# Kernel tuning notes

Hardware: AMD Instinct MI355X
Metric: run time of the kernel (lower is better)

Reference implementation:

```python
import jax, jax.numpy as jnp
import numpy as np

ROUTING_ITERS = 3


def _squash(x):
    # scale = |x|^2 / (1+|x|^2) ; out = scale * x / |x|  (matches torch module exactly)
    squared_norm = jnp.sum(x * x, axis=-1, keepdims=True)
    scale = squared_norm / (1.0 + squared_norm)
    return scale * x / jnp.sqrt(squared_norm)


def setup_inputs() -> dict:
    key = jax.random.key(0)
    k1, k2 = jax.random.split(key)
    B, NODES, CIN = 64, 6272, 8
    CAPS, COUT = 10, 16
    x = jax.random.normal(k1, (B, NODES, CIN), dtype=jnp.float32)
    W = jax.random.normal(k2, (CAPS, NODES, CIN, COUT), dtype=jnp.float32)
    return {"x": x, "W": W}


def reference(x, W):
    # u_hat: [B, caps, nodes, 1, out]  (the torch code's per-node 1x8 @ 8x16 matmul)
    u_hat = jnp.einsum('bni,cnio->bcno', x, W)[:, :, :, None, :]
    b_ij = jnp.zeros_like(u_hat)
    v_j = None
    for it in range(ROUTING_ITERS):
        c_ij = jax.nn.softmax(b_ij, axis=2)  # softmax over nodes dim (dim=2)
        s_j = jnp.sum(c_ij * u_hat, axis=2, keepdims=True)  # [B,caps,1,1,out]
        v_j = _squash(s_j)
        if it < ROUTING_ITERS - 1:
            a_ij = jnp.sum(u_hat * v_j, axis=-1, keepdims=True)  # agreement
            b_ij = b_ij + a_ij  # broadcasts over the out dim, as in torch
    return jnp.squeeze(v_j, axis=3)  # [B, caps, 1, out]
```

## Files before the change

### kernel.cpp

```cpp
#include <hip/hip_runtime.h>
#include <math.h>

#define NODES 6272
#define BATCH 64
#define NCAPS 10
#define CIN   8
#define COUT  16
#define NWB   16
#define NWW   4
#define CHUNKS (NODES / NWB)
#define PART_STRIDE 20

__global__ __launch_bounds__(256) void k_xpose(const float* __restrict__ x,
                                               float* __restrict__ xT) {
    int g = blockIdx.x * 256 + threadIdx.x;
    int b = g & 63;
    int n = g >> 6;
    const float* xp = x + (size_t)b * (NODES * CIN) + (size_t)n * CIN;
    float4 a0 = *reinterpret_cast<const float4*>(xp);
    float4 a1 = *reinterpret_cast<const float4*>(xp + 4);
    float4* op = reinterpret_cast<float4*>(xT + (size_t)g * 8);
    op[0] = a0;
    op[1] = a1;
}

template<int PASS>
__global__ __launch_bounds__(256) void k_pass(const float* __restrict__ xT,
                                              const float* __restrict__ W,
                                              const float* __restrict__ vsum,
                                              float* __restrict__ part) {
    __shared__ float Wl[NWB * 128];
    __shared__ float Rbuf[2][64][PART_STRIDE];

    int bid  = blockIdx.x;
    int wid  = threadIdx.x >> 6;
    int lane = threadIdx.x & 63;
    int c    = bid % NCAPS;
    int ch   = bid / NCAPS;
    int n0   = ch * NWB;

    {
        const float4* src = reinterpret_cast<const float4*>(
            W + ((size_t)c * NODES + n0) * (CIN * COUT));
        float4* dst = reinterpret_cast<float4*>(Wl);
        int t = threadIdx.x;
        dst[t]       = src[t];
        dst[t + 256] = src[t + 256];
    }

    float vs[COUT];
    if (PASS > 0) {
        const float* vp = vsum + ((size_t)(c * BATCH) + lane) * COUT;
        #pragma unroll
        for (int o = 0; o < COUT; ++o) vs[o] = vp[o];
    }

    __syncthreads();

    float acc[COUT];
    #pragma unroll
    for (int o = 0; o < COUT; ++o) acc[o] = 0.f;
    float z = 0.f;

    int nbase = wid * NWW;
    #pragma unroll 2
    for (int nn = 0; nn < NWW; ++nn) {
        int nl = nbase + nn;
        int n  = n0 + nl;

        const float4* xp = reinterpret_cast<const float4*>(xT + ((size_t)n * 64 + lane) * 8);
        float4 xa = xp[0], xb = xp[1];
        float xv[8] = {xa.x, xa.y, xa.z, xa.w, xb.x, xb.y, xb.z, xb.w};

        const float4* wl = reinterpret_cast<const float4*>(Wl + nl * 128);

        float u[COUT];
        #pragma unroll
        for (int o = 0; o < COUT; ++o) u[o] = 0.f;
        #pragma unroll
        for (int i = 0; i < CIN; ++i) {
            float xi = xv[i];
            float4 w0 = wl[i * 4 + 0];
            float4 w1 = wl[i * 4 + 1];
            float4 w2 = wl[i * 4 + 2];
            float4 w3 = wl[i * 4 + 3];
            u[0]  = fmaf(xi, w0.x, u[0]);  u[1]  = fmaf(xi, w0.y, u[1]);
            u[2]  = fmaf(xi, w0.z, u[2]);  u[3]  = fmaf(xi, w0.w, u[3]);
            u[4]  = fmaf(xi, w1.x, u[4]);  u[5]  = fmaf(xi, w1.y, u[5]);
            u[6]  = fmaf(xi, w1.z, u[6]);  u[7]  = fmaf(xi, w1.w, u[7]);
            u[8]  = fmaf(xi, w2.x, u[8]);  u[9]  = fmaf(xi, w2.y, u[9]);
            u[10] = fmaf(xi, w2.z, u[10]); u[11] = fmaf(xi, w2.w, u[11]);
            u[12] = fmaf(xi, w3.x, u[12]); u[13] = fmaf(xi, w3.y, u[13]);
            u[14] = fmaf(xi, w3.z, u[14]); u[15] = fmaf(xi, w3.w, u[15]);
        }

        if (PASS == 0) {
            #pragma unroll
            for (int o = 0; o < COUT; ++o) acc[o] += u[o];
            z += 1.f;
        } else {
            float lg = 0.f;
            #pragma unroll
            for (int o = 0; o < COUT; ++o) lg = fmaf(u[o], vs[o], lg);
            float w = __expf(lg);
            z += w;
            #pragma unroll
            for (int o = 0; o < COUT; ++o) acc[o] = fmaf(w, u[o], acc[o]);
        }
    }

    if (wid >= 2) {
        float* rp = &Rbuf[wid - 2][lane][0];
        #pragma unroll
        for (int q = 0; q < 4; ++q)
            reinterpret_cast<float4*>(rp)[q] =
                make_float4(acc[q*4+0], acc[q*4+1], acc[q*4+2], acc[q*4+3]);
        rp[16] = z;
    }
    __syncthreads();
    if (wid < 2) {
        const float* rp = &Rbuf[wid][lane][0];
        #pragma unroll
        for (int o = 0; o < COUT; ++o) acc[o] += rp[o];
        z += rp[16];
    }
    __syncthreads();
    if (wid == 1) {
        float* rp = &Rbuf[0][lane][0];
        #pragma unroll
        for (int q = 0; q < 4; ++q)
            reinterpret_cast<float4*>(rp)[q] =
                make_float4(acc[q*4+0], acc[q*4+1], acc[q*4+2], acc[q*4+3]);
        rp[16] = z;
    }
    __syncthreads();
    if (wid == 0) {
        const float* rp = &Rbuf[0][lane][0];
        #pragma unroll
        for (int o = 0; o < COUT; ++o) acc[o] += rp[o];
        z += rp[16];

        float* pp = part + ((size_t)bid * BATCH + lane) * PART_STRIDE;
        #pragma unroll
        for (int q = 0; q < 4; ++q)
            reinterpret_cast<float4*>(pp)[q] =
                make_float4(acc[q*4+0], acc[q*4+1], acc[q*4+2], acc[q*4+3]);
        pp[16] = z;
    }
}

template<int PASS>
__global__ __launch_bounds__(256) void k_merge(const float* __restrict__ part,
                                               float* __restrict__ vsum,
                                               float* __restrict__ out) {
    __shared__ float R[3][PART_STRIDE];
    int bid = blockIdx.x;
    int c = bid >> 6;
    int b = bid & 63;
    int t = threadIdx.x;

    float a[COUT];
    #pragma unroll
    for (int o = 0; o < COUT; ++o) a[o] = 0.f;
    float z = 0.f;

    for (int ch = t; ch < CHUNKS; ch += 256) {
        const float* pp = part + ((size_t)(ch * NCAPS + c) * BATCH + b) * PART_STRIDE;
        float4 q0 = reinterpret_cast<const float4*>(pp)[0];
        float4 q1 = reinterpret_cast<const float4*>(pp)[1];
        float4 q2 = reinterpret_cast<const float4*>(pp)[2];
        float4 q3 = reinterpret_cast<const float4*>(pp)[3];
        a[0]+=q0.x; a[1]+=q0.y; a[2]+=q0.z; a[3]+=q0.w;
        a[4]+=q1.x; a[5]+=q1.y; a[6]+=q1.z; a[7]+=q1.w;
        a[8]+=q2.x; a[9]+=q2.y; a[10]+=q2.z; a[11]+=q2.w;
        a[12]+=q3.x; a[13]+=q3.y; a[14]+=q3.z; a[15]+=q3.w;
        z += pp[16];
    }

    #pragma unroll
    for (int off = 32; off >= 1; off >>= 1) {
        z += __shfl_xor(z, off);
        #pragma unroll
        for (int o = 0; o < COUT; ++o) a[o] += __shfl_xor(a[o], off);
    }

    int wid = t >> 6, lane = t & 63;
    if (lane == 0 && wid > 0) {
        #pragma unroll
        for (int o = 0; o < COUT; ++o) R[wid - 1][o] = a[o];
        R[wid - 1][16] = z;
    }
    __syncthreads();
    if (t == 0) {
        #pragma unroll
        for (int r = 0; r < 3; ++r) {
            #pragma unroll
            for (int o = 0; o < COUT; ++o) a[o] += R[r][o];
            z += R[r][16];
        }
        float s[COUT];
        float sn = 0.f;
        #pragma unroll
        for (int o = 0; o < COUT; ++o) { s[o] = a[o] / z; sn += s[o] * s[o]; }
        float scale = sn / ((1.f + sn) * sqrtf(sn));
        if (PASS == 0) {
            float* vp = vsum + ((size_t)(c * BATCH) + b) * COUT;
            #pragma unroll
            for (int o = 0; o < COUT; ++o) vp[o] = scale * s[o];
        } else if (PASS == 1) {
            float* vp = vsum + ((size_t)(c * BATCH) + b) * COUT;
            #pragma unroll
            for (int o = 0; o < COUT; ++o) vp[o] += scale * s[o];
        } else {
            float* op = out + ((size_t)(b * NCAPS + c)) * COUT;
            #pragma unroll
            for (int o = 0; o < COUT; ++o) op[o] = scale * s[o];
        }
    }
}

extern "C" void kernel_launch(void* const* d_in, const int* in_sizes, int n_in,
                              void* d_out, int out_size, void* d_ws, size_t ws_size,
                              hipStream_t stream) {
    const float* x = (const float*)d_in[0];
    const float* W = (const float*)d_in[1];
    float* out = (float*)d_out;
    float* ws  = (float*)d_ws;

    float* xT   = ws;
    float* part = ws + (size_t)NODES * BATCH * CIN;
    float* vsum = part + (size_t)NCAPS * CHUNKS * BATCH * PART_STRIDE;

    k_xpose<<<(NODES * BATCH) / 256, 256, 0, stream>>>(x, xT);

    k_pass<0><<<NCAPS * CHUNKS, 256, 0, stream>>>(xT, W, vsum, part);
    k_merge<0><<<NCAPS * BATCH, 256, 0, stream>>>(part, vsum, out);

    k_pass<1><<<NCAPS * CHUNKS, 256, 0, stream>>>(xT, W, vsum, part);
    k_merge<1><<<NCAPS * BATCH, 256, 0, stream>>>(part, vsum, out);

    k_pass<2><<<NCAPS * CHUNKS, 256, 0, stream>>>(xT, W, vsum, part);
    k_merge<2><<<NCAPS * BATCH, 256, 0, stream>>>(part, vsum, out);
}
```

Measured before the change: 205.2 us.

## Split output dimension across half-waves and read W directly from global

Each wave now handles 32 batch rows with the 16 output features split between two half-waves of 8. The logit dot product is combined across the halves with a shuffle. The LDS staging of W and its barrier are removed, so W is read straight from global memory, with all lanes in a half-wave reading the same address (a broadcast). The intra-block reduction drops from three barrier stages to one. This halves per-thread registers and accumulator work and shortens the reduction, at the cost of more global/L1 traffic for W and an extra shuffle per node.

Measured after the change: 327.2 us. +59.5%, slower.

```diff
diff --git a/kernel.cpp b/kernel.cpp
--- a/kernel.cpp
+++ b/kernel.cpp
@@ -7,7 +7,6 @@
 #define CIN   8
 #define COUT  16
 #define NWB   16
-#define NWW   4
 #define CHUNKS (NODES / NWB)
 #define PART_STRIDE 20
 
@@ -29,123 +28,89 @@
                                               const float* __restrict__ W,
                                               const float* __restrict__ vsum,
                                               float* __restrict__ part) {
-    __shared__ float Wl[NWB * 128];
-    __shared__ float Rbuf[2][64][PART_STRIDE];
+    __shared__ float Rbuf[2][32][PART_STRIDE];
 
     int bid  = blockIdx.x;
-    int wid  = threadIdx.x >> 6;
+    int w    = threadIdx.x >> 6;
+    int bh   = w & 1;
+    int ws   = w >> 1;
     int lane = threadIdx.x & 63;
+    int bl   = lane & 31;
+    int oh   = lane >> 5;
+    int b    = bh * 32 + bl;
     int c    = bid % NCAPS;
     int ch   = bid / NCAPS;
     int n0   = ch * NWB;
 
-    {
-        const float4* src = reinterpret_cast<const float4*>(
-            W + ((size_t)c * NODES + n0) * (CIN * COUT));
-        float4* dst = reinterpret_cast<float4*>(Wl);
-        int t = threadIdx.x;
-        dst[t]       = src[t];
-        dst[t + 256] = src[t + 256];
-    }
-
-    float vs[COUT];
+    float vs[8];
     if (PASS > 0) {
-        const float* vp = vsum + ((size_t)(c * BATCH) + lane) * COUT;
-        #pragma unroll
-        for (int o = 0; o < COUT; ++o) vs[o] = vp[o];
-    }
-
-    __syncthreads();
-
-    float acc[COUT];
+        const float* vp = vsum + ((size_t)(c * BATCH) + b) * COUT + oh * 8;
+        #pragma unroll
+        for (int j = 0; j < 8; ++j) vs[j] = vp[j];
+    }
+
+    float acc[8];
     #pragma unroll
-    for (int o = 0; o < COUT; ++o) acc[o] = 0.f;
+    for (int j = 0; j < 8; ++j) acc[j] = 0.f;
     float z = 0.f;
 
-    int nbase = wid * NWW;
     #pragma unroll 2
-    for (int nn = 0; nn < NWW; ++nn) {
-        int nl = nbase + nn;
-        int n  = n0 + nl;
-
-        const float4* xp = reinterpret_cast<const float4*>(xT + ((size_t)n * 64 + lane) * 8);
+    for (int nn = ws; nn < NWB; nn += 2) {
+        int n = n0 + nn;
+
+        const float4* xp = reinterpret_cast<const float4*>(xT + ((size_t)n * 64 + b) * 8);
         float4 xa = xp[0], xb = xp[1];
         float xv[8] = {xa.x, xa.y, xa.z, xa.w, xb.x, xb.y, xb.z, xb.w};
 
-        const float4* wl = reinterpret_cast<const float4*>(Wl + nl * 128);
-
-        float u[COUT];
-        #pragma unroll
-        for (int o = 0; o < COUT; ++o) u[o] = 0.f;
+        const float* wp = W + ((size_t)c * NODES + n) * (CIN * COUT) + oh * 8;
+
+        float u[8];
+        #pragma unroll
+        for (int j = 0; j < 8; ++j) u[j] = 0.f;
         #pragma unroll
         for (int i = 0; i < CIN; ++i) {
+            float4 w0 = *reinterpret_cast<const float4*>(wp + i * COUT);
+            float4 w1 = *reinterpret_cast<const float4*>(wp + i * COUT + 4);
             float xi = xv[i];
-            float4 w0 = wl[i * 4 + 0];
-            float4 w1 = wl[i * 4 + 1];
-            float4 w2 = wl[i * 4 + 2];
-            float4 w3 = wl[i * 4 + 3];
-            u[0]  = fmaf(xi, w0.x, u[0]);  u[1]  = fmaf(xi, w0.y, u[1]);
-            u[2]  = fmaf(xi, w0.z, u[2]);  u[3]  = fmaf(xi, w0.w, u[3]);
-            u[4]  = fmaf(xi, w1.x, u[4]);  u[5]  = fmaf(xi, w1.y, u[5]);
-            u[6]  = fmaf(xi, w1.z, u[6]);  u[7]  = fmaf(xi, w1.w, u[7]);
-            u[8]  = fmaf(xi, w2.x, u[8]);  u[9]  = fmaf(xi, w2.y, u[9]);
-            u[10] = fmaf(xi, w2.z, u[10]); u[11] = fmaf(xi, w2.w, u[11]);
-            u[12] = fmaf(xi, w3.x, u[12]); u[13] = fmaf(xi, w3.y, u[13]);
-            u[14] = fmaf(xi, w3.z, u[14]); u[15] = fmaf(xi, w3.w, u[15]);
+            u[0] = fmaf(xi, w0.x, u[0]);  u[1] = fmaf(xi, w0.y, u[1]);
+            u[2] = fmaf(xi, w0.z, u[2]);  u[3] = fmaf(xi, w0.w, u[3]);
+            u[4] = fmaf(xi, w1.x, u[4]);  u[5] = fmaf(xi, w1.y, u[5]);
+            u[6] = fmaf(xi, w1.z, u[6]);  u[7] = fmaf(xi, w1.w, u[7]);
         }
 
         if (PASS == 0) {
             #pragma unroll
-            for (int o = 0; o < COUT; ++o) acc[o] += u[o];
+            for (int j = 0; j < 8; ++j) acc[j] += u[j];
             z += 1.f;
         } else {
             float lg = 0.f;
             #pragma unroll
-            for (int o = 0; o < COUT; ++o) lg = fmaf(u[o], vs[o], lg);
-            float w = __expf(lg);
-            z += w;
-            #pragma unroll
-            for (int o = 0; o < COUT; ++o) acc[o] = fmaf(w, u[o], acc[o]);
-        }
-    }
-
-    if (wid >= 2) {
-        float* rp = &Rbuf[wid - 2][lane][0];
-        #pragma unroll
-        for (int q = 0; q < 4; ++q)
-            reinterpret_cast<float4*>(rp)[q] =
-                make_float4(acc[q*4+0], acc[q*4+1], acc[q*4+2], acc[q*4+3]);
-        rp[16] = z;
+            for (int j = 0; j < 8; ++j) lg = fmaf(u[j], vs[j], lg);
+            lg += __shfl_xor(lg, 32);
+            float wgt = __expf(lg);
+            z += wgt;
+            #pragma unroll
+            for (int j = 0; j < 8; ++j) acc[j] = fmaf(wgt, u[j], acc[j]);
+        }
+    }
+
+    if (ws == 1) {
+        float* rp = &Rbuf[bh][bl][oh * 8];
+        reinterpret_cast<float4*>(rp)[0] = make_float4(acc[0], acc[1], acc[2], acc[3]);
+        reinterpret_cast<float4*>(rp)[1] = make_float4(acc[4], acc[5], acc[6], acc[7]);
+        if (oh == 0) Rbuf[bh][bl][16] = z;
     }
     __syncthreads();
-    if (wid < 2) {
-        const float* rp = &Rbuf[wid][lane][0];
-        #pragma unroll
-        for (int o = 0; o < COUT; ++o) acc[o] += rp[o];
-        z += rp[16];
-    }
-    __syncthreads();
-    if (wid == 1) {
-        float* rp = &Rbuf[0][lane][0];
-        #pragma unroll
-        for (int q = 0; q < 4; ++q)
-            reinterpret_cast<float4*>(rp)[q] =
-                make_float4(acc[q*4+0], acc[q*4+1], acc[q*4+2], acc[q*4+3]);
-        rp[16] = z;
-    }
-    __syncthreads();
-    if (wid == 0) {
-        const float* rp = &Rbuf[0][lane][0];
-        #pragma unroll
-        for (int o = 0; o < COUT; ++o) acc[o] += rp[o];
-        z += rp[16];
-
-        float* pp = part + ((size_t)bid * BATCH + lane) * PART_STRIDE;
-        #pragma unroll
-        for (int q = 0; q < 4; ++q)
-            reinterpret_cast<float4*>(pp)[q] =
-                make_float4(acc[q*4+0], acc[q*4+1], acc[q*4+2], acc[q*4+3]);
-        pp[16] = z;
+    if (ws == 0) {
+        const float* rp = &Rbuf[bh][bl][oh * 8];
+        #pragma unroll
+        for (int j = 0; j < 8; ++j) acc[j] += rp[j];
+        z += Rbuf[bh][bl][16];
+
+        float* pp = part + ((size_t)bid * BATCH + b) * PART_STRIDE + oh * 8;
+        reinterpret_cast<float4*>(pp)[0] = make_float4(acc[0], acc[1], acc[2], acc[3]);
+        reinterpret_cast<float4*>(pp)[1] = make_float4(acc[4], acc[5], acc[6], acc[7]);
+        if (oh == 0) pp[16] = z;
     }
 }
 
```
